# Kernel tuning notes

Hardware: AMD Instinct MI355X
Metric: run time of the kernel (lower is better)

The kernel has to match this reference:

```python
import jax, jax.numpy as jnp
import numpy as np

B, S, E, H = 2, 2048, 1024, 16
HD = E // H


def setup_inputs() -> dict:
    key = jax.random.key(0)
    ks = jax.random.split(key, 5)
    scale = 1.0 / np.sqrt(E)
    return {
        "x": jax.random.normal(ks[0], (B, S, E), dtype=jnp.float32),
        "Wq": jax.random.normal(ks[1], (H, HD, E), dtype=jnp.float32) * scale,
        "Wk": jax.random.normal(ks[2], (H, HD, E), dtype=jnp.float32) * scale,
        "Wv": jax.random.normal(ks[3], (H, HD, E), dtype=jnp.float32) * scale,
        "Wo": jax.random.normal(ks[4], (E, E), dtype=jnp.float32) * scale,
    }


def reference(x, Wq, Wk, Wv, Wo):
    # Batched per-head projections: torch Linear y = x @ W.T, W: [head_dim, E]
    q = jnp.einsum("bse,hde->bshd", x, Wq)  # [B,S,H,HD]
    k = jnp.einsum("bse,hde->bshd", x, Wk)
    v = jnp.einsum("bse,hde->bshd", x, Wv)
    # Scaled dot-product attention; original scales by sqrt(head_dim)
    scores = jnp.einsum("bqhd,bkhd->bhqk", q, k) / jnp.sqrt(jnp.float32(HD))
    attn = jax.nn.softmax(scores, axis=-1)  # [B,H,S,S]
    out_h = jnp.einsum("bhqk,bkhd->bqhd", attn, v)  # [B,S,H,HD]
    out_cat = out_h.reshape(x.shape[0], x.shape[1], -1)  # concat heads -> [B,S,E]
    return out_cat @ Wo.T
```

## Files before the change

kernel.cpp:

```cpp
#include <hip/hip_runtime.h>
#include <hip/hip_bf16.h>

typedef unsigned short u16;
typedef unsigned int u32;
typedef __attribute__((ext_vector_type(4))) float f32x4;
typedef __attribute__((ext_vector_type(8))) short short8;
typedef __attribute__((ext_vector_type(8))) unsigned short u16x8;
typedef __attribute__((ext_vector_type(4))) unsigned short u16x4;
typedef __attribute__((ext_vector_type(2))) unsigned int u32x2;

#define BATCH 2
#define SEQ   2048
#define EMB   1024
#define NH    16
#define HD    64

__device__ inline u16 f2bf(float f) {
    unsigned u = __builtin_bit_cast(unsigned, f);
    unsigned r = u + 0x7FFFu + ((u >> 16) & 1u);
    return (u16)(r >> 16);
}

__device__ inline float fexp2(float x) {
    float r;
    asm("v_exp_f32 %0, %1" : "=v"(r) : "v"(x));
    return r;
}

__device__ inline void gload16(const void* g, void* l) {
    __builtin_amdgcn_global_load_lds(
        (const __attribute__((address_space(1))) unsigned int*)g,
        (__attribute__((address_space(3))) unsigned int*)l, 16, 0, 0);
}

__global__ __launch_bounds__(256) void convert_all(
    const float* __restrict__ x,
    const float* __restrict__ Wq, const float* __restrict__ Wk, const float* __restrict__ Wv,
    u16* __restrict__ Xb, u16* __restrict__ Wqkv)
{
    const long gidx = (long)blockIdx.x * 2048 + (long)threadIdx.x * 8;
    const float* src;
    u16* dst;
    if (gidx < 4194304L) {
        src = x + gidx; dst = Xb + gidx;
    } else {
        const long r = gidx - 4194304L;
        const int w = (int)(r >> 20);
        const long off = r & 1048575L;
        src = (w == 0 ? Wq : w == 1 ? Wk : Wv) + off;
        dst = Wqkv + r;
    }
    f32x4 a = *(const f32x4*)src;
    f32x4 b = *(const f32x4*)(src + 4);
    u16x8 o;
    #pragma unroll
    for (int j = 0; j < 4; ++j) { o[j] = f2bf(a[j]); o[4 + j] = f2bf(b[j]); }
    *(u16x8*)dst = o;
}

__global__ __launch_bounds__(256) void convert_wo(
    const float* __restrict__ Wo, u16* __restrict__ Wob)
{
    const long gidx = (long)blockIdx.x * 2048 + (long)threadIdx.x * 8;
    f32x4 a = *(const f32x4*)(Wo + gidx);
    f32x4 b = *(const f32x4*)(Wo + gidx + 4);
    u16x8 o;
    #pragma unroll
    for (int j = 0; j < 4; ++j) { o[j] = f2bf(a[j]); o[4 + j] = f2bf(b[j]); }
    *(u16x8*)(Wob + gidx) = o;
}

template<int MODE>
__global__ __launch_bounds__(256) void gemm_bt(
    const u16* __restrict__ A, const u16* __restrict__ Bb,
    u16* __restrict__ Qo, u16* __restrict__ Ko, u16* __restrict__ VTo,
    float* __restrict__ Fo)
{
    __shared__ u16 As[2][128 * 64];
    __shared__ u16 Bs[2][128 * 64];

    const int tid = threadIdx.x;
    const int m0 = blockIdx.x * 128;
    const int n0 = blockIdx.y * 128;

    const int lane = tid & 63;
    const int lr = lane & 15;
    const int lg = lane >> 4;
    const int wid = tid >> 6;
    const int wm = wid >> 1, wn = wid & 1;

    const int grow = lane >> 3;
    const int gcolb = ((lane & 7) ^ grow) << 4;
    const int rswz = (lr & 7);

    f32x4 acc[4][4] = {};

    auto issue = [&](int kt, int buf) {
        const int k0b = kt * 128;
        #pragma unroll
        for (int t = 0; t < 4; ++t) {
            const int row = (wid * 4 + t) * 8 + grow;
            gload16((const char*)A + (size_t)(m0 + row) * 2048 + k0b + gcolb,
                    (char*)As[buf] + (wid * 4 + t) * 1024);
            gload16((const char*)Bb + (size_t)(n0 + row) * 2048 + k0b + gcolb,
                    (char*)Bs[buf] + (wid * 4 + t) * 1024);
        }
    };

    issue(0, 0);

    for (int kt = 0; kt < 16; ++kt) {
        const int cur = kt & 1;
        __syncthreads();
        if (kt + 1 < 16) issue(kt + 1, cur ^ 1);

        const u16* Ac = As[cur];
        const u16* Bc = Bs[cur];
        #pragma unroll
        for (int kk = 0; kk < 2; ++kk) {
            short8 a[4], b[4];
            #pragma unroll
            for (int i = 0; i < 4; ++i)
                a[i] = *(const short8*)((const char*)Ac + (wm * 64 + i * 16 + lr) * 128
                                        + (((kk * 4 + lg) ^ rswz) << 4));
            #pragma unroll
            for (int i = 0; i < 4; ++i)
                b[i] = *(const short8*)((const char*)Bc + (wn * 64 + i * 16 + lr) * 128
                                        + (((kk * 4 + lg) ^ rswz) << 4));
            #pragma unroll
            for (int mi = 0; mi < 4; ++mi)
                #pragma unroll
                for (int ni = 0; ni < 4; ++ni)
                    acc[mi][ni] = __builtin_amdgcn_mfma_f32_16x16x32_bf16(a[mi], b[ni], acc[mi][ni], 0, 0, 0);
        }
    }

    const int mb = m0 + wm * 64;
    const int nb = n0 + wn * 64;
    if (MODE == 0) {
        const int w = n0 >> 10;
        const float qs = (w == 0) ? 0.125f * 1.44269504f : 1.0f;
        #pragma unroll
        for (int mi = 0; mi < 4; ++mi) {
            #pragma unroll
            for (int ni = 0; ni < 4; ++ni) {
                const int m = mb + mi * 16 + lg * 4;
                const int nn = (nb + ni * 16 + lr) & 1023;
                const int h = nn >> 6, d = nn & 63;
                const int bb = m >> 11, s = m & 2047;
                const size_t bh = (size_t)(bb * NH + h);
                if (w == 2) {
                    u16x4 v;
                    #pragma unroll
                    for (int i = 0; i < 4; ++i) v[i] = f2bf(acc[mi][ni][i]);
                    *(u16x4*)&VTo[(bh * HD + d) * SEQ + s] = v;
                } else {
                    u16* P = (w == 0) ? Qo : Ko;
                    #pragma unroll
                    for (int i = 0; i < 4; ++i)
                        P[(bh * SEQ + s + i) * HD + d] = f2bf(acc[mi][ni][i] * qs);
                }
            }
        }
    } else {
        #pragma unroll
        for (int mi = 0; mi < 4; ++mi)
            #pragma unroll
            for (int ni = 0; ni < 4; ++ni) {
                const int m = mb + mi * 16 + lg * 4;
                const int n = nb + ni * 16 + lr;
                #pragma unroll
                for (int i = 0; i < 4; ++i)
                    Fo[(size_t)(m + i) * EMB + n] = acc[mi][ni][i];
            }
    }
}

__global__ __launch_bounds__(512) void attn_fwd(
    const u16* __restrict__ Q, const u16* __restrict__ K,
    const u16* __restrict__ VT, u16* __restrict__ Cat)
{
    __shared__ u16 Ks[2][64 * 64];
    __shared__ u16 Vs[2][80 * 64];
    __shared__ u16 PT[8][16 * 72];

    const int tid = threadIdx.x;
    const int lane = tid & 63;
    const int lr = lane & 15;
    const int lg = lane >> 4;
    const int wid = tid >> 6;
    const int qt = blockIdx.x;
    const int bh = blockIdx.y;
    const int b = bh >> 4, h = bh & 15;

    if (tid < 128) {
        const int row = 64 + (tid >> 3), sl = tid & 7;
        u16x8 ones;
        #pragma unroll
        for (int j = 0; j < 8; ++j) ones[j] = 0x3F80;
        *(u16x8*)((char*)Vs[0] + row * 128 + ((sl ^ (row & 7)) << 4)) = ones;
        *(u16x8*)((char*)Vs[1] + row * 128 + ((sl ^ (row & 7)) << 4)) = ones;
    }

    const u16* Qg = Q + ((size_t)bh * SEQ + qt * 128 + wid * 16 + lr) * HD;
    short8 qf[2];
    qf[0] = *(const short8*)(Qg + lg * 8);
    qf[1] = *(const short8*)(Qg + 32 + lg * 8);

    float m = -1e30f;
    f32x4 accO[5] = {};

    const u16* Kg = K + (size_t)bh * SEQ * HD;
    const u16* Vg = VT + (size_t)bh * HD * SEQ;

    const int srow = lane >> 3;
    const int schunk = ((lane & 7) ^ srow) << 4;

    auto issueKV = [&](int nt, int buf) {
        const int kv0 = nt * 64;
        const int krow = wid * 8 + srow;
        gload16((const char*)Kg + (size_t)(kv0 + krow) * 128 + schunk,
                (char*)Ks[buf] + wid * 1024);
        gload16((const char*)Vg + (size_t)krow * (SEQ * 2) + kv0 * 2 + schunk,
                (char*)Vs[buf] + wid * 1024);
    };

    issueKV(0, 0);

    for (int nt = 0; nt < SEQ / 64; ++nt) {
        const int cur = nt & 1;
        __syncthreads();
        if (nt + 1 < SEQ / 64) issueKV(nt + 1, cur ^ 1);

        f32x4 st[4] = {};
        #pragma unroll
        for (int kk = 0; kk < 2; ++kk) {
            const short8 qv = qf[kk];
            #pragma unroll
            for (int c = 0; c < 4; ++c) {
                const short8 kf = *(const short8*)((const char*)Ks[cur] + (c * 16 + lr) * 128
                                                   + (((kk * 4 + lg) ^ (lr & 7)) << 4));
                st[c] = __builtin_amdgcn_mfma_f32_16x16x32_bf16(kf, qv, st[c], 0, 0, 0);
            }
        }

        float mx = fmaxf(
            fmaxf(fmaxf(fmaxf(st[0][0], st[0][1]), fmaxf(st[0][2], st[0][3])),
                  fmaxf(fmaxf(st[1][0], st[1][1]), fmaxf(st[1][2], st[1][3]))),
            fmaxf(fmaxf(fmaxf(st[2][0], st[2][1]), fmaxf(st[2][2], st[2][3])),
                  fmaxf(fmaxf(st[3][0], st[3][1]), fmaxf(st[3][2], st[3][3]))));
        mx = fmaxf(mx, __shfl_xor(mx, 16));
        mx = fmaxf(mx, __shfl_xor(mx, 32));
        if (!__all(mx - m <= 11.5f)) {
            const float nm = fmaxf(m, mx);
            const float corr = fexp2(m - nm);
            m = nm;
            #pragma unroll
            for (int dc = 0; dc < 5; ++dc)
                accO[dc] *= corr;
        }
        #pragma unroll
        for (int c = 0; c < 4; ++c)
            #pragma unroll
            for (int i = 0; i < 4; ++i)
                st[c][i] = fexp2(st[c][i] - m);

        #pragma unroll
        for (int c = 0; c < 4; ++c) {
            u32 w0, w1;
            asm("v_cvt_pk_bf16_f32 %0, %1, %2" : "=v"(w0) : "v"(st[c][0]), "v"(st[c][1]));
            asm("v_cvt_pk_bf16_f32 %0, %1, %2" : "=v"(w1) : "v"(st[c][2]), "v"(st[c][3]));
            u32x2 pk; pk[0] = w0; pk[1] = w1;
            *(u32x2*)&PT[wid][lr * 72 + c * 16 + lg * 4] = pk;
        }
        asm volatile("s_waitcnt lgkmcnt(0)" ::: "memory");
        __builtin_amdgcn_sched_barrier(0);

        #pragma unroll
        for (int kk = 0; kk < 2; ++kk) {
            const short8 pf = *(const short8*)&PT[wid][lr * 72 + kk * 32 + lg * 8];
            #pragma unroll
            for (int dc = 0; dc < 5; ++dc) {
                const short8 vf = *(const short8*)((const char*)Vs[cur] + (dc * 16 + lr) * 128
                                                   + (((kk * 4 + lg) ^ (lr & 7)) << 4));
                accO[dc] = __builtin_amdgcn_mfma_f32_16x16x32_bf16(vf, pf, accO[dc], 0, 0, 0);
            }
        }
    }

    const float invl = 1.f / accO[4][0];
    const int qs = qt * 128 + wid * 16 + lr;
    u16* ob = Cat + (size_t)b * SEQ * EMB + (size_t)qs * EMB + h * HD;
    #pragma unroll
    for (int dc = 0; dc < 4; ++dc) {
        u16x4 o;
        #pragma unroll
        for (int i = 0; i < 4; ++i) o[i] = f2bf(accO[dc][i] * invl);
        *(u16x4*)&ob[dc * 16 + lg * 4] = o;
    }
}

extern "C" void kernel_launch(void* const* d_in, const int* in_sizes, int n_in,
                              void* d_out, int out_size, void* d_ws, size_t ws_size,
                              hipStream_t stream) {
    const float* x  = (const float*)d_in[0];
    const float* Wq = (const float*)d_in[1];
    const float* Wk = (const float*)d_in[2];
    const float* Wv = (const float*)d_in[3];
    const float* Wo = (const float*)d_in[4];
    float* out = (float*)d_out;

    u16* Xb   = (u16*)d_out;
    u16* Wqkv = (u16*)d_out + (size_t)4 * 1048576;

    char* ws = (char*)d_ws;
    u16* Qb  = (u16*)(ws);
    u16* Kb  = (u16*)(ws + (size_t)8  * 1048576);
    u16* VTb = (u16*)(ws + (size_t)16 * 1048576);
    u16* Cat = (u16*)(ws + (size_t)24 * 1048576);
    u16* Wob = Qb;

    convert_all<<<3584, 256, 0, stream>>>(x, Wq, Wk, Wv, Xb, Wqkv);

    dim3 g1(4096 / 128, 3072 / 128);
    gemm_bt<0><<<g1, 256, 0, stream>>>(Xb, Wqkv, Qb, Kb, VTb, nullptr);

    dim3 g2(SEQ / 128, BATCH * NH);
    attn_fwd<<<g2, 512, 0, stream>>>(Qb, Kb, VTb, Cat);

    convert_wo<<<512, 256, 0, stream>>>(Wo, Wob);
    dim3 g3(4096 / 128, 1024 / 128);
    gemm_bt<1><<<g3, 256, 0, stream>>>(Cat, Wob, nullptr, nullptr, nullptr, out);
}
```

Before: 130.4 us.

## Replace QKV projection GEMM with 256x256-tile 8-wave kernel

Adds a dedicated QKV projection GEMM that uses 256x256 output tiles with 512 threads, a BK=64 double-buffered LDS pipeline, and staged fragment loads interleaved with MFMA groups under setprio. The larger tile raises arithmetic intensity and cuts global and LDS traffic per FLOP, at the cost of fewer blocks (192) and heavier register and LDS use, 128KB per block. The old gemm_bt now serves only the output projection, so its QKV epilogue branch is removed.

```diff
diff --git a/kernel.cpp b/kernel.cpp
--- a/kernel.cpp
+++ b/kernel.cpp
@@ -70,6 +70,154 @@
     *(u16x8*)(Wob + gidx) = o;
 }
 
+__global__ __launch_bounds__(512, 2) void gemm256(
+    const u16* __restrict__ A, const u16* __restrict__ Bb,
+    u16* __restrict__ Qo, u16* __restrict__ Ko, u16* __restrict__ VTo)
+{
+    __shared__ u16 As[2][256 * 64];
+    __shared__ u16 Bs[2][256 * 64];
+
+    const int tid = threadIdx.x;
+    const int lane = tid & 63;
+    const int wid = tid >> 6;
+    const int lr = lane & 15;
+    const int lg = lane >> 4;
+    const int wr = wid >> 2;
+    const int wc = wid & 3;
+    const int m0 = blockIdx.x * 256;
+    const int n0 = blockIdx.y * 256;
+
+    const int grow = lane >> 3;
+    const int schunk = ((lane & 7) ^ grow) << 4;
+
+    auto issueTile = [&](int kt, int buf) {
+        const int k0b = kt * 128;
+        #pragma unroll
+        for (int i = 0; i < 4; ++i) {
+            const int row = i * 64 + wid * 8 + grow;
+            gload16((const char*)A + (size_t)(m0 + row) * 2048 + k0b + schunk,
+                    (char*)As[buf] + i * 8192 + wid * 1024);
+            gload16((const char*)Bb + (size_t)(n0 + row) * 2048 + k0b + schunk,
+                    (char*)Bs[buf] + i * 8192 + wid * 1024);
+        }
+    };
+
+    issueTile(0, 0);
+    issueTile(1, 1);
+
+    f32x4 acc[8][4] = {};
+    const int rsw = (lr & 7);
+
+    for (int t = 0; t < 16; ++t) {
+        if (t < 15) { asm volatile("s_waitcnt vmcnt(8)" ::: "memory"); }
+        else        { asm volatile("s_waitcnt vmcnt(0)" ::: "memory"); }
+        __builtin_amdgcn_sched_barrier(0);
+        __builtin_amdgcn_s_barrier();
+        __builtin_amdgcn_sched_barrier(0);
+
+        const u16* Ac = As[t & 1];
+        const u16* Bc = Bs[t & 1];
+
+        short8 a[4][2], b0[2][2], b1[2][2];
+
+        #pragma unroll
+        for (int fi = 0; fi < 4; ++fi)
+            #pragma unroll
+            for (int ks = 0; ks < 2; ++ks)
+                a[fi][ks] = *(const short8*)((const char*)Ac + (wr * 128 + fi * 16 + lr) * 128
+                                             + (((ks * 4 + lg) ^ rsw) << 4));
+        #pragma unroll
+        for (int fj = 0; fj < 2; ++fj)
+            #pragma unroll
+            for (int ks = 0; ks < 2; ++ks)
+                b0[fj][ks] = *(const short8*)((const char*)Bc + (wc * 64 + fj * 16 + lr) * 128
+                                              + (((ks * 4 + lg) ^ rsw) << 4));
+        __builtin_amdgcn_s_setprio(1);
+        #pragma unroll
+        for (int fi = 0; fi < 4; ++fi)
+            #pragma unroll
+            for (int fj = 0; fj < 2; ++fj)
+                #pragma unroll
+                for (int ks = 0; ks < 2; ++ks)
+                    acc[fi][fj] = __builtin_amdgcn_mfma_f32_16x16x32_bf16(a[fi][ks], b0[fj][ks], acc[fi][fj], 0, 0, 0);
+        __builtin_amdgcn_s_setprio(0);
+
+        #pragma unroll
+        for (int fj = 0; fj < 2; ++fj)
+            #pragma unroll
+            for (int ks = 0; ks < 2; ++ks)
+                b1[fj][ks] = *(const short8*)((const char*)Bc + (wc * 64 + (fj + 2) * 16 + lr) * 128
+                                              + (((ks * 4 + lg) ^ rsw) << 4));
+        __builtin_amdgcn_s_setprio(1);
+        #pragma unroll
+        for (int fi = 0; fi < 4; ++fi)
+            #pragma unroll
+            for (int fj = 0; fj < 2; ++fj)
+                #pragma unroll
+                for (int ks = 0; ks < 2; ++ks)
+                    acc[fi][fj + 2] = __builtin_amdgcn_mfma_f32_16x16x32_bf16(a[fi][ks], b1[fj][ks], acc[fi][fj + 2], 0, 0, 0);
+        __builtin_amdgcn_s_setprio(0);
+
+        #pragma unroll
+        for (int fi = 0; fi < 4; ++fi)
+            #pragma unroll
+            for (int ks = 0; ks < 2; ++ks)
+                a[fi][ks] = *(const short8*)((const char*)Ac + (wr * 128 + (fi + 4) * 16 + lr) * 128
+                                             + (((ks * 4 + lg) ^ rsw) << 4));
+        __builtin_amdgcn_s_setprio(1);
+        #pragma unroll
+        for (int fi = 0; fi < 4; ++fi)
+            #pragma unroll
+            for (int fj = 0; fj < 2; ++fj)
+                #pragma unroll
+                for (int ks = 0; ks < 2; ++ks)
+                    acc[fi + 4][fj + 2] = __builtin_amdgcn_mfma_f32_16x16x32_bf16(a[fi][ks], b1[fj][ks], acc[fi + 4][fj + 2], 0, 0, 0);
+        __builtin_amdgcn_s_setprio(0);
+
+        __builtin_amdgcn_s_setprio(1);
+        #pragma unroll
+        for (int fi = 0; fi < 4; ++fi)
+            #pragma unroll
+            for (int fj = 0; fj < 2; ++fj)
+                #pragma unroll
+                for (int ks = 0; ks < 2; ++ks)
+                    acc[fi + 4][fj] = __builtin_amdgcn_mfma_f32_16x16x32_bf16(a[fi][ks], b0[fj][ks], acc[fi + 4][fj], 0, 0, 0);
+        __builtin_amdgcn_s_setprio(0);
+
+        __builtin_amdgcn_sched_barrier(0);
+        __builtin_amdgcn_s_barrier();
+        __builtin_amdgcn_sched_barrier(0);
+        if (t + 2 < 16) issueTile(t + 2, t & 1);
+    }
+
+    const int w = n0 >> 10;
+    const float qs = (w == 0) ? 0.125f * 1.44269504f : 1.0f;
+    const int mb = m0 + wr * 128;
+    const int nb = n0 + wc * 64;
+    #pragma unroll
+    for (int fi = 0; fi < 8; ++fi) {
+        #pragma unroll
+        for (int fj = 0; fj < 4; ++fj) {
+            const int m = mb + fi * 16 + lg * 4;
+            const int nn = (nb + fj * 16 + lr) & 1023;
+            const int h = nn >> 6, d = nn & 63;
+            const int bb = m >> 11, s = m & 2047;
+            const size_t bh = (size_t)(bb * NH + h);
+            if (w == 2) {
+                u16x4 v;
+                #pragma unroll
+                for (int i = 0; i < 4; ++i) v[i] = f2bf(acc[fi][fj][i]);
+                *(u16x4*)&VTo[(bh * HD + d) * SEQ + s] = v;
+            } else {
+                u16* P = (w == 0) ? Qo : Ko;
+                #pragma unroll
+                for (int i = 0; i < 4; ++i)
+                    P[(bh * SEQ + s + i) * HD + d] = f2bf(acc[fi][fj][i] * qs);
+            }
+        }
+    }
+}
+
 template<int MODE>
 __global__ __launch_bounds__(256) void gemm_bt(
     const u16* __restrict__ A, const u16* __restrict__ Bb,
@@ -137,43 +285,16 @@
 
     const int mb = m0 + wm * 64;
     const int nb = n0 + wn * 64;
-    if (MODE == 0) {
-        const int w = n0 >> 10;
-        const float qs = (w == 0) ? 0.125f * 1.44269504f : 1.0f;
-        #pragma unroll
-        for (int mi = 0; mi < 4; ++mi) {
-            #pragma unroll
-            for (int ni = 0; ni < 4; ++ni) {
-                const int m = mb + mi * 16 + lg * 4;
-                const int nn = (nb + ni * 16 + lr) & 1023;
-                const int h = nn >> 6, d = nn & 63;
-                const int bb = m >> 11, s = m & 2047;
-                const size_t bh = (size_t)(bb * NH + h);
-                if (w == 2) {
-                    u16x4 v;
-                    #pragma unroll
-                    for (int i = 0; i < 4; ++i) v[i] = f2bf(acc[mi][ni][i]);
-                    *(u16x4*)&VTo[(bh * HD + d) * SEQ + s] = v;
-                } else {
-                    u16* P = (w == 0) ? Qo : Ko;
-                    #pragma unroll
-                    for (int i = 0; i < 4; ++i)
-                        P[(bh * SEQ + s + i) * HD + d] = f2bf(acc[mi][ni][i] * qs);
-                }
-            }
-        }
-    } else {
-        #pragma unroll
-        for (int mi = 0; mi < 4; ++mi)
-            #pragma unroll
-            for (int ni = 0; ni < 4; ++ni) {
-                const int m = mb + mi * 16 + lg * 4;
-                const int n = nb + ni * 16 + lr;
-                #pragma unroll
-                for (int i = 0; i < 4; ++i)
-                    Fo[(size_t)(m + i) * EMB + n] = acc[mi][ni][i];
-            }
-    }
+    #pragma unroll
+    for (int mi = 0; mi < 4; ++mi)
+        #pragma unroll
+        for (int ni = 0; ni < 4; ++ni) {
+            const int m = mb + mi * 16 + lg * 4;
+            const int n = nb + ni * 16 + lr;
+            #pragma unroll
+            for (int i = 0; i < 4; ++i)
+                Fo[(size_t)(m + i) * EMB + n] = acc[mi][ni][i];
+        }
 }
 
 __global__ __launch_bounds__(512) void attn_fwd(
@@ -322,8 +443,8 @@
 
     convert_all<<<3584, 256, 0, stream>>>(x, Wq, Wk, Wv, Xb, Wqkv);
 
-    dim3 g1(4096 / 128, 3072 / 128);
-    gemm_bt<0><<<g1, 256, 0, stream>>>(Xb, Wqkv, Qb, Kb, VTb, nullptr);
+    dim3 g1(4096 / 256, 3072 / 256);
+    gemm256<<<g1, 512, 0, stream>>>(Xb, Wqkv, Qb, Kb, VTb);
 
     dim3 g2(SEQ / 128, BATCH * NH);
     attn_fwd<<<g2, 512, 0, stream>>>(Qb, Kb, VTb, Cat);
```

After: 126.0 us. 1.04x faster.
